# Kernel tuning notes

Measured on AMD Instinct MI355X. Metric: run time of the kernel, lower is better.

The kernel has to match this reference:

```python
import jax, jax.numpy as jnp
import numpy as np

N_NODES = 100000
N_EDGES = 1000000
D_FEAT = 64


def setup_inputs() -> dict:
    key = jax.random.key(0)
    k1, k2, k3 = jax.random.split(key, 3)
    features = jax.random.normal(k1, (N_NODES, D_FEAT), dtype=jnp.float32)
    src = jax.random.randint(k2, (N_EDGES,), 0, N_NODES, dtype=jnp.int64)
    dst = jax.random.randint(k3, (N_EDGES,), 0, N_NODES, dtype=jnp.int64)
    return {"features": features, "src": src, "dst": dst}


def reference(features, src, dst):
    # DGL update_all(copy_u('h','m'), sum('m','h')):
    # out[v] = sum_{(u,v) in E} features[u]
    msgs = features[src]  # [E, D] gather of source node features
    h = jax.ops.segment_sum(msgs, dst, num_segments=N_NODES)  # [N, D] scatter-add
    return h
```

## Files before the change

kernel.cpp:

```cpp
#include <hip/hip_runtime.h>


#define N_NODES   100000
#define N_EDGES   1000000
#define D_FEAT    64
#define NPB       128
#define NPB_SHIFT 7
#define NB        782
#define PAD       32
#define EPB       8192
#define MAXP      4096

__global__ void zero_ints_kernel(int* __restrict__ p, int n) {
    int i = blockIdx.x * blockDim.x + threadIdx.x;
    if (i < n) p[i] = 0;
}

__global__ __launch_bounds__(512) void hist_kernel(const int* __restrict__ dst,
                                                   int* __restrict__ gcounts, int n) {
    __shared__ int cnt[NB];
    for (int i = threadIdx.x; i < NB; i += 512) cnt[i] = 0;
    __syncthreads();
    int base = blockIdx.x * EPB + threadIdx.x * 4;
#pragma unroll
    for (int step = 0; step < 4; ++step) {
        int idx = base + step * 2048;
        if (idx < n) {
            int4 d = *reinterpret_cast<const int4*>(dst + idx);
            atomicAdd(&cnt[d.x >> NPB_SHIFT], 1);
            atomicAdd(&cnt[d.y >> NPB_SHIFT], 1);
            atomicAdd(&cnt[d.z >> NPB_SHIFT], 1);
            atomicAdd(&cnt[d.w >> NPB_SHIFT], 1);
        }
    }
    __syncthreads();
    for (int b = threadIdx.x; b < NB; b += 512)
        if (cnt[b]) atomicAdd(&gcounts[b * PAD], cnt[b]);
}

__global__ __launch_bounds__(1024) void scan_kernel(const int* __restrict__ gcounts,
                                                    int* __restrict__ bases,
                                                    int* __restrict__ gcursor, int n_edges) {
    __shared__ int lds[1024];
    int t = threadIdx.x;
    int v = (t < NB) ? gcounts[t * PAD] : 0;
    lds[t] = v;
    __syncthreads();
    for (int off = 1; off < 1024; off <<= 1) {
        int u = (t >= off) ? lds[t - off] : 0;
        __syncthreads();
        lds[t] += u;
        __syncthreads();
    }
    if (t < NB) { int b = lds[t] - v; bases[t] = b; gcursor[t * PAD] = b; }
    if (t == 0) bases[NB] = n_edges;
}

__global__ __launch_bounds__(512) void partition_kernel(const int* __restrict__ src,
                                                        const int* __restrict__ dst,
                                                        int* __restrict__ gcursor,
                                                        int* __restrict__ pairs, int n) {
    __shared__ int cnt[NB];
    __shared__ int lbase[NB];
    for (int i = threadIdx.x; i < NB; i += 512) cnt[i] = 0;
    __syncthreads();

    int base = blockIdx.x * EPB + threadIdx.x * 4;
    int4 s[4], d[4];
    bool valid[4];
#pragma unroll
    for (int step = 0; step < 4; ++step) {
        int idx = base + step * 2048;
        valid[step] = (idx < n);
        if (valid[step]) {
            s[step] = *reinterpret_cast<const int4*>(src + idx);
            d[step] = *reinterpret_cast<const int4*>(dst + idx);
            atomicAdd(&cnt[d[step].x >> NPB_SHIFT], 1);
            atomicAdd(&cnt[d[step].y >> NPB_SHIFT], 1);
            atomicAdd(&cnt[d[step].z >> NPB_SHIFT], 1);
            atomicAdd(&cnt[d[step].w >> NPB_SHIFT], 1);
        }
    }
    __syncthreads();
    for (int b = threadIdx.x; b < NB; b += 512) {
        int c = cnt[b];
        lbase[b] = c ? atomicAdd(&gcursor[b * PAD], c) : 0;
    }
    __syncthreads();
    for (int b = threadIdx.x; b < NB; b += 512) cnt[b] = 0;
    __syncthreads();
#pragma unroll
    for (int step = 0; step < 4; ++step) {
        if (valid[step]) {
            int b, p;
            b = d[step].x >> NPB_SHIFT; p = atomicAdd(&cnt[b], 1); pairs[lbase[b] + p] = (s[step].x << NPB_SHIFT) | (d[step].x & (NPB - 1));
            b = d[step].y >> NPB_SHIFT; p = atomicAdd(&cnt[b], 1); pairs[lbase[b] + p] = (s[step].y << NPB_SHIFT) | (d[step].y & (NPB - 1));
            b = d[step].z >> NPB_SHIFT; p = atomicAdd(&cnt[b], 1); pairs[lbase[b] + p] = (s[step].z << NPB_SHIFT) | (d[step].z & (NPB - 1));
            b = d[step].w >> NPB_SHIFT; p = atomicAdd(&cnt[b], 1); pairs[lbase[b] + p] = (s[step].w << NPB_SHIFT) | (d[step].w & (NPB - 1));
        }
    }
}

__global__ __launch_bounds__(512) void gather_kernel(const float* __restrict__ feat,
                                                     const int* __restrict__ bases,
                                                     const int* __restrict__ pairs,
                                                     float* __restrict__ out,
                                                     int n_nodes) {
    __shared__ int pbuf[MAXP];
    __shared__ int sorted[MAXP];
    __shared__ int deg[NPB];
    __shared__ int sc[NPB];
    __shared__ int start[NPB + 1];
    __shared__ int cur[NPB];

    int b = blockIdx.x, t = threadIdx.x;
    int lane = t & 63, wave = t >> 6;
    int lo = bases[b], hi = bases[b + 1];
    int node0 = b * NPB;

    bool first = true;
    for (int c = lo; c < hi || first; c += MAXP) {
        int n = hi - c;
        if (n > MAXP) n = MAXP;
        if (n < 0) n = 0;

        if (t < NPB) deg[t] = 0;
        __syncthreads();
        for (int i = t; i < n; i += 512) {
            int p = pairs[c + i];
            pbuf[i] = p;
            atomicAdd(&deg[p & (NPB - 1)], 1);
        }
        __syncthreads();
        if (t < NPB) sc[t] = deg[t];
        __syncthreads();
        for (int off = 1; off < NPB; off <<= 1) {
            int u = (t < NPB && t >= off) ? sc[t - off] : 0;
            __syncthreads();
            if (t < NPB) sc[t] += u;
            __syncthreads();
        }
        if (t < NPB) { start[t + 1] = sc[t]; cur[t] = sc[t] - deg[t]; }
        if (t == 0) start[0] = 0;
        __syncthreads();
        for (int i = t; i < n; i += 512) {
            int p = pbuf[i];
            int r = p & (NPB - 1);
            int pos = atomicAdd(&cur[r], 1);
            sorted[pos] = p >> NPB_SHIFT;
        }
        __syncthreads();

        for (int r = wave; r < NPB; r += 8) {
            int s0 = start[r], e0 = start[r + 1];
            float acc = 0.f;
            int i = s0;
            for (; i + 3 < e0; i += 4) {
                int i0 = sorted[i], i1 = sorted[i + 1], i2 = sorted[i + 2], i3 = sorted[i + 3];
                float v0 = feat[(size_t)i0 * D_FEAT + lane];
                float v1 = feat[(size_t)i1 * D_FEAT + lane];
                float v2 = feat[(size_t)i2 * D_FEAT + lane];
                float v3 = feat[(size_t)i3 * D_FEAT + lane];
                acc += v0 + v1 + v2 + v3;
            }
            for (; i < e0; ++i) acc += feat[(size_t)sorted[i] * D_FEAT + lane];

            int node = node0 + r;
            if (node < n_nodes) {
                float* o = out + (size_t)node * D_FEAT + lane;
                if (first) *o = acc;
                else atomicAdd(o, acc);
            }
        }
        first = false;
        __syncthreads();
    }
}

extern "C" void kernel_launch(void* const* d_in, const int* in_sizes, int n_in,
                              void* d_out, int out_size, void* d_ws, size_t ws_size,
                              hipStream_t stream) {
    const float* feat = (const float*)d_in[0];
    const int*   src  = (const int*)d_in[1];
    const int*   dst  = (const int*)d_in[2];
    float*       out  = (float*)d_out;

    const int n_edges = in_sizes[1];

    int* gcounts = (int*)d_ws;
    int* gcursor = gcounts + NB * PAD;
    int* bases   = gcursor + NB * PAD;
    int* pairs   = bases + NB + 1;

    int nzero = NB * PAD;
    zero_ints_kernel<<<(nzero + 255) / 256, 256, 0, stream>>>(gcounts, nzero);

    int pblocks = (n_edges + EPB - 1) / EPB;
    hist_kernel<<<pblocks, 512, 0, stream>>>(dst, gcounts, n_edges);
    scan_kernel<<<1, 1024, 0, stream>>>(gcounts, bases, gcursor, n_edges);
    partition_kernel<<<pblocks, 512, 0, stream>>>(src, dst, gcursor, pairs, n_edges);
    gather_kernel<<<NB, 512, 0, stream>>>(feat, bases, pairs, out, N_NODES);
}
```

Measured before the change: 76.36 us.

## Fuse scan into histogram, double edges per block, float4 gather lanes

The separate scan kernel is removed: the last histogram block, found with an atomic done counter, performs the prefix scan, which saves one launch. Edges per block for the histogram and partition kernels are doubled, halving the grid and the number of global atomics at the cost of more registers per thread. The gather now has each wave process four edges at once with float4 loads per 16-lane group and combines the partial sums with shuffles, which raises memory-level parallelism per row. The trade-off is more reduction work, and float atomics are split into four scalar adds on the overflow path.

Result: slower. 81.08 us (+6.2%).

```diff
diff --git a/kernel.cpp b/kernel.cpp
--- a/kernel.cpp
+++ b/kernel.cpp
@@ -8,22 +8,27 @@
 #define NPB_SHIFT 7
 #define NB        782
 #define PAD       32
-#define EPB       8192
+#define EPB       16384
 #define MAXP      4096
 
-__global__ void zero_ints_kernel(int* __restrict__ p, int n) {
+__global__ void zero_ints_kernel(int* __restrict__ p, int* __restrict__ done, int n) {
     int i = blockIdx.x * blockDim.x + threadIdx.x;
     if (i < n) p[i] = 0;
-}
-
-__global__ __launch_bounds__(512) void hist_kernel(const int* __restrict__ dst,
-                                                   int* __restrict__ gcounts, int n) {
+    if (i == 0) *done = 0;
+}
+
+__global__ __launch_bounds__(512) void hist_scan_kernel(const int* __restrict__ dst,
+                                                        int* __restrict__ gcounts,
+                                                        int* __restrict__ bases,
+                                                        int* __restrict__ gcursor,
+                                                        int* __restrict__ done, int n) {
     __shared__ int cnt[NB];
+    __shared__ int isLast;
     for (int i = threadIdx.x; i < NB; i += 512) cnt[i] = 0;
     __syncthreads();
     int base = blockIdx.x * EPB + threadIdx.x * 4;
 #pragma unroll
-    for (int step = 0; step < 4; ++step) {
+    for (int step = 0; step < 8; ++step) {
         int idx = base + step * 2048;
         if (idx < n) {
             int4 d = *reinterpret_cast<const int4*>(dst + idx);
@@ -36,24 +41,32 @@
     __syncthreads();
     for (int b = threadIdx.x; b < NB; b += 512)
         if (cnt[b]) atomicAdd(&gcounts[b * PAD], cnt[b]);
-}
-
-__global__ __launch_bounds__(1024) void scan_kernel(const int* __restrict__ gcounts,
-                                                    int* __restrict__ bases,
-                                                    int* __restrict__ gcursor, int n_edges) {
-    __shared__ int lds[1024];
+
+    __syncthreads();
+    __threadfence();
+    if (threadIdx.x == 0) isLast = (atomicAdd(done, 1) == (int)gridDim.x - 1);
+    __syncthreads();
+    if (!isLast) return;
+
     int t = threadIdx.x;
-    int v = (t < NB) ? gcounts[t * PAD] : 0;
-    lds[t] = v;
-    __syncthreads();
-    for (int off = 1; off < 1024; off <<= 1) {
-        int u = (t >= off) ? lds[t - off] : 0;
-        __syncthreads();
-        lds[t] += u;
-        __syncthreads();
-    }
-    if (t < NB) { int b = lds[t] - v; bases[t] = b; gcursor[t * PAD] = b; }
-    if (t == 0) bases[NB] = n_edges;
+    int b0 = 2 * t, b1 = 2 * t + 1;
+    int a0 = (b0 < NB) ? __hip_atomic_load(&gcounts[b0 * PAD], __ATOMIC_RELAXED,
+                                           __HIP_MEMORY_SCOPE_AGENT) : 0;
+    int a1 = (b1 < NB) ? __hip_atomic_load(&gcounts[b1 * PAD], __ATOMIC_RELAXED,
+                                           __HIP_MEMORY_SCOPE_AGENT) : 0;
+    int s = a0 + a1;
+    cnt[t] = s;
+    __syncthreads();
+    for (int off = 1; off < 512; off <<= 1) {
+        int u = (t >= off) ? cnt[t - off] : 0;
+        __syncthreads();
+        cnt[t] += u;
+        __syncthreads();
+    }
+    int excl = cnt[t] - s;
+    if (b0 < NB) { bases[b0] = excl;      gcursor[b0 * PAD] = excl; }
+    if (b1 < NB) { bases[b1] = excl + a0; gcursor[b1 * PAD] = excl + a0; }
+    if (t == 511) bases[NB] = cnt[511];
 }
 
 __global__ __launch_bounds__(512) void partition_kernel(const int* __restrict__ src,
@@ -66,10 +79,10 @@
     __syncthreads();
 
     int base = blockIdx.x * EPB + threadIdx.x * 4;
-    int4 s[4], d[4];
-    bool valid[4];
+    int4 s[8], d[8];
+    bool valid[8];
 #pragma unroll
-    for (int step = 0; step < 4; ++step) {
+    for (int step = 0; step < 8; ++step) {
         int idx = base + step * 2048;
         valid[step] = (idx < n);
         if (valid[step]) {
@@ -90,7 +103,7 @@
     for (int b = threadIdx.x; b < NB; b += 512) cnt[b] = 0;
     __syncthreads();
 #pragma unroll
-    for (int step = 0; step < 4; ++step) {
+    for (int step = 0; step < 8; ++step) {
         if (valid[step]) {
             int b, p;
             b = d[step].x >> NPB_SHIFT; p = atomicAdd(&cnt[b], 1); pairs[lbase[b] + p] = (s[step].x << NPB_SHIFT) | (d[step].x & (NPB - 1));
@@ -115,6 +128,7 @@
 
     int b = blockIdx.x, t = threadIdx.x;
     int lane = t & 63, wave = t >> 6;
+    int g = lane >> 4, l16 = lane & 15;
     int lo = bases[b], hi = bases[b + 1];
     int node0 = b * NPB;
 
@@ -145,31 +159,36 @@
         __syncthreads();
         for (int i = t; i < n; i += 512) {
             int p = pbuf[i];
-            int r = p & (NPB - 1);
-            int pos = atomicAdd(&cur[r], 1);
+            int pos = atomicAdd(&cur[p & (NPB - 1)], 1);
             sorted[pos] = p >> NPB_SHIFT;
         }
         __syncthreads();
 
         for (int r = wave; r < NPB; r += 8) {
             int s0 = start[r], e0 = start[r + 1];
-            float acc = 0.f;
-            int i = s0;
-            for (; i + 3 < e0; i += 4) {
-                int i0 = sorted[i], i1 = sorted[i + 1], i2 = sorted[i + 2], i3 = sorted[i + 3];
-                float v0 = feat[(size_t)i0 * D_FEAT + lane];
-                float v1 = feat[(size_t)i1 * D_FEAT + lane];
-                float v2 = feat[(size_t)i2 * D_FEAT + lane];
-                float v3 = feat[(size_t)i3 * D_FEAT + lane];
-                acc += v0 + v1 + v2 + v3;
+            float4 acc = {0.f, 0.f, 0.f, 0.f};
+            for (int i = s0; i < e0; i += 4) {
+                if (g < e0 - i) {
+                    int sn = sorted[i + g];
+                    const float4 v = *reinterpret_cast<const float4*>(
+                        feat + (size_t)sn * D_FEAT + l16 * 4);
+                    acc.x += v.x; acc.y += v.y; acc.z += v.z; acc.w += v.w;
+                }
             }
-            for (; i < e0; ++i) acc += feat[(size_t)sorted[i] * D_FEAT + lane];
+            acc.x += __shfl_xor(acc.x, 16); acc.y += __shfl_xor(acc.y, 16);
+            acc.z += __shfl_xor(acc.z, 16); acc.w += __shfl_xor(acc.w, 16);
+            acc.x += __shfl_xor(acc.x, 32); acc.y += __shfl_xor(acc.y, 32);
+            acc.z += __shfl_xor(acc.z, 32); acc.w += __shfl_xor(acc.w, 32);
 
             int node = node0 + r;
-            if (node < n_nodes) {
-                float* o = out + (size_t)node * D_FEAT + lane;
-                if (first) *o = acc;
-                else atomicAdd(o, acc);
+            if (node < n_nodes && lane < 16) {
+                float* o = out + (size_t)node * D_FEAT + l16 * 4;
+                if (first) {
+                    *reinterpret_cast<float4*>(o) = acc;
+                } else {
+                    atomicAdd(o + 0, acc.x); atomicAdd(o + 1, acc.y);
+                    atomicAdd(o + 2, acc.z); atomicAdd(o + 3, acc.w);
+                }
             }
         }
         first = false;
@@ -190,14 +209,14 @@
     int* gcounts = (int*)d_ws;
     int* gcursor = gcounts + NB * PAD;
     int* bases   = gcursor + NB * PAD;
-    int* pairs   = bases + NB + 1;
+    int* done    = bases + NB + 1;
+    int* pairs   = done + 1;
 
     int nzero = NB * PAD;
-    zero_ints_kernel<<<(nzero + 255) / 256, 256, 0, stream>>>(gcounts, nzero);
+    zero_ints_kernel<<<(nzero + 255) / 256, 256, 0, stream>>>(gcounts, done, nzero);
 
     int pblocks = (n_edges + EPB - 1) / EPB;
-    hist_kernel<<<pblocks, 512, 0, stream>>>(dst, gcounts, n_edges);
-    scan_kernel<<<1, 1024, 0, stream>>>(gcounts, bases, gcursor, n_edges);
+    hist_scan_kernel<<<pblocks, 512, 0, stream>>>(dst, gcounts, bases, gcursor, done, n_edges);
     partition_kernel<<<pblocks, 512, 0, stream>>>(src, dst, gcursor, pairs, n_edges);
     gather_kernel<<<NB, 512, 0, stream>>>(feat, bases, pairs, out, N_NODES);
 }
```
